# Kernel optimization log

Measured on AMD Instinct MI355X. Metric: run time of the kernel, lower is better.

## Reference

```python
import jax, jax.numpy as jnp
import numpy as np
import math

B, S, HID = 2, 2048, 2048
NH, NKV, HD = 32, 8, 64
THETA = 10000.0
EPS = 1e-6
LAYER_IDX = 1
LAMBDA_INIT = 0.8 - 0.6 * math.exp(-0.3 * LAYER_IDX)
LAMBDA_STD = 0.1


def setup_inputs() -> dict:
    key = jax.random.key(0)
    ks = jax.random.split(key, 10)
    hidden_states = jax.random.normal(ks[0], (B, S, HID), jnp.float32)
    # RoPE cos/sin, llama convention: emb = cat(freqs, freqs)
    inv_freq = 1.0 / (THETA ** (np.arange(0, HD, 2, dtype=np.float32) / HD))
    freqs = np.outer(np.arange(S, dtype=np.float32), inv_freq)  # [S, HD/2]
    emb = np.concatenate([freqs, freqs], axis=-1)                # [S, HD]
    cos = jnp.broadcast_to(jnp.asarray(np.cos(emb), jnp.float32)[None], (B, S, HD))
    sin = jnp.broadcast_to(jnp.asarray(np.sin(emb), jnp.float32)[None], (B, S, HD))
    # additive causal mask [B,1,S,S]
    causal = jnp.triu(jnp.full((S, S), -1e9, dtype=jnp.float32), k=1)
    attention_mask = jnp.broadcast_to(causal[None, None], (B, 1, S, S))
    sc = 0.02
    wq = sc * jax.random.normal(ks[1], (NH * HD, HID), jnp.float32)
    wk = sc * jax.random.normal(ks[2], (NKV * HD, HID), jnp.float32)
    wv = sc * jax.random.normal(ks[3], (NKV * HD, HID), jnp.float32)
    wo = sc * jax.random.normal(ks[4], (HID, NH * HD), jnp.float32)
    lambda_q1 = LAMBDA_STD * jax.random.normal(ks[5], (HD,), jnp.float32)
    lambda_k1 = LAMBDA_STD * jax.random.normal(ks[6], (HD,), jnp.float32)
    lambda_q2 = LAMBDA_STD * jax.random.normal(ks[7], (HD,), jnp.float32)
    lambda_k2 = LAMBDA_STD * jax.random.normal(ks[8], (HD,), jnp.float32)
    return {"hidden_states": hidden_states, "cos": cos, "sin": sin,
            "attention_mask": attention_mask, "wq": wq, "wk": wk, "wv": wv,
            "wo": wo, "lambda_q1": lambda_q1, "lambda_k1": lambda_k1,
            "lambda_q2": lambda_q2, "lambda_k2": lambda_k2}


def _rotate_half(x):
    x1, x2 = jnp.split(x, 2, axis=-1)
    return jnp.concatenate([-x2, x1], axis=-1)


def reference(hidden_states, cos, sin, attention_mask, wq, wk, wv, wo,
              lambda_q1, lambda_k1, lambda_q2, lambda_k2):
    b, s, _ = hidden_states.shape
    # projections -> [b, h, s, d]
    q = jnp.einsum('bsh,oh->bso', hidden_states, wq).reshape(b, s, NH, HD).transpose(0, 2, 1, 3)
    k = jnp.einsum('bsh,oh->bso', hidden_states, wk).reshape(b, s, NKV, HD).transpose(0, 2, 1, 3)
    v = jnp.einsum('bsh,oh->bso', hidden_states, wv).reshape(b, s, NKV, HD).transpose(0, 2, 1, 3)
    # rotary
    c, sn = cos[:, None], sin[:, None]  # [b,1,s,d]
    q = q * c + _rotate_half(q) * sn
    k = k * c + _rotate_half(k) * sn
    # GQA repeat
    groups = NH // NKV
    k = jnp.repeat(k, groups, axis=1)
    v = jnp.repeat(v, groups, axis=1)
    # diff-attention value trick: pair head i with head i+NH/2 -> [b, NH, s, 2d]
    v = jnp.concatenate([v[:, :NH // 2], v[:, NH // 2:]], axis=-1)  # [b, NH/2, s, 2d]
    v = jnp.concatenate([v, v], axis=1)                              # [b, NH, s, 2d]
    # scores + causal mask, stable softmax in fp32
    aw = jnp.einsum('bhqd,bhkd->bhqk', q, k) / math.sqrt(HD)
    aw = aw + attention_mask
    aw = jax.nn.softmax(aw.astype(jnp.float32), axis=-1).astype(q.dtype)
    ao = jnp.einsum('bhqk,bhkd->bhqd', aw, v)  # [b, NH, s, 2d]
    lam1 = jnp.exp(jnp.sum((lambda_q1 * lambda_k1).astype(jnp.float32)))
    lam2 = jnp.exp(jnp.sum((lambda_q2 * lambda_k2).astype(jnp.float32)))
    lam = (lam1 - lam2).astype(q.dtype) + LAMBDA_INIT
    a1, a2 = ao[:, :NH // 2], ao[:, NH // 2:]
    out = a1 - lam * a2  # [b, NH/2, s, 2d]
    # RMSNorm over last dim (no affine)
    out = out * jax.lax.rsqrt(jnp.mean(out * out, axis=-1, keepdims=True) + EPS)
    out = (1.0 - LAMBDA_INIT) * out
    out = out.transpose(0, 2, 1, 3).reshape(b, s, NH * HD)
    return jnp.einsum('bso,ho->bsh', out, wo)
```

## Files before the change

### kernel.cpp

```cpp
#include <hip/hip_runtime.h>

typedef __attribute__((ext_vector_type(8))) short bhalf8;
typedef __attribute__((ext_vector_type(4))) float floatx4;

constexpr int B_ = 2, S_ = 2048, HID_ = 2048, NH_ = 32, NKV_ = 8, HD_ = 64;
constexpr float LAMBDA_INIT_F = 0.35550906759096924f;
constexpr float EPS_ = 1e-6f;
constexpr float QSCALE_ = 0.18033688011112042f;

#define DEVINL __device__ __forceinline__

DEVINL float bf2f(unsigned short u) {
    union { unsigned u; float f; } v; v.u = ((unsigned)u) << 16; return v.f;
}
DEVINL unsigned short f2bf(float f) {
    union { float f; unsigned u; } v; v.f = f;
    unsigned u = v.u;
    return (unsigned short)((u + 0x7fffu + ((u >> 16) & 1u)) >> 16);
}
DEVINL float fexp2(float x) {
#if __has_builtin(__builtin_amdgcn_exp2f)
    return __builtin_amdgcn_exp2f(x);
#else
    return exp2f(x);
#endif
}
DEVINL unsigned pk_bf16(float a, float b) {
#if __has_builtin(__builtin_amdgcn_cvt_pk_bf16_f32)
    typedef __bf16 bf16x2_t __attribute__((ext_vector_type(2)));
    bf16x2_t p = __builtin_amdgcn_cvt_pk_bf16_f32(a, b);
    unsigned r;
    __builtin_memcpy(&r, &p, 4);
    return r;
#else
    return (unsigned)f2bf(a) | ((unsigned)f2bf(b) << 16);
#endif
}
DEVINL void load_lds16(const unsigned short* g, unsigned short* l) {
    __builtin_amdgcn_global_load_lds(
        (const __attribute__((address_space(1))) unsigned int*)g,
        (__attribute__((address_space(3))) unsigned int*)l, 16, 0, 0);
}

__global__ __launch_bounds__(256)
void cvt_all(const float* __restrict__ hs, const float* __restrict__ wq,
             const float* __restrict__ wk, const float* __restrict__ wv,
             const float* __restrict__ wo, unsigned short* __restrict__ hs_bf,
             unsigned short* __restrict__ wcat, unsigned short* __restrict__ wo_bf) {
    const size_t i = (size_t)(blockIdx.x * 256 + threadIdx.x) * 4;
    const float* src;
    unsigned short* dst;
    size_t off;
    float scale = 1.f;
    if (i < 8388608) { src = hs; dst = hs_bf; off = 0; }
    else if (i < 12582912) { src = wq; dst = wcat; off = 8388608; scale = QSCALE_; }
    else if (i < 13631488) { src = wk; dst = wcat + 4194304; off = 12582912; }
    else if (i < 14680064) { src = wv; dst = wcat + 5242880; off = 13631488; }
    else { src = wo; dst = wo_bf; off = 14680064; }
    const size_t k = i - off;
    const float4 v = *(const float4*)(src + k);
    ushort4 o;
    o.x = f2bf(v.x * scale); o.y = f2bf(v.y * scale);
    o.z = f2bf(v.z * scale); o.w = f2bf(v.w * scale);
    *(ushort4*)(dst + k) = o;
}

__global__ void lam_kernel(const float* __restrict__ q1, const float* __restrict__ k1,
                           const float* __restrict__ q2, const float* __restrict__ k2,
                           float* __restrict__ lam) {
    const int l = threadIdx.x;
    float p1 = q1[l] * k1[l];
    float p2 = q2[l] * k2[l];
    #pragma unroll
    for (int off = 1; off < 64; off <<= 1) {
        p1 += __shfl_xor(p1, off, 64);
        p2 += __shfl_xor(p2, off, 64);
    }
    if (l == 0) *lam = expf(p1) - expf(p2) + LAMBDA_INIT_F;
}

__global__ __launch_bounds__(256)
void gemm_qkv(const unsigned short* __restrict__ A, const unsigned short* __restrict__ Bw,
              const float* __restrict__ cosb, const float* __restrict__ sinb,
              unsigned short* __restrict__ Qr, unsigned short* __restrict__ Kr,
              unsigned short* __restrict__ VT) {
    constexpr int K = 2048;
    union GS {
        struct { unsigned short A[2][128][32]; unsigned short B[2][128][32]; } d;
        unsigned short vt[128][130];
    };
    __shared__ __align__(16) GS gsm;
    const int t = threadIdx.x;
    const int w = t >> 6, lane = t & 63, quad = lane >> 4, lid = lane & 15;
    const int wr = (w >> 1) * 64, wc = (w & 1) * 64;
    const long bm = (long)blockIdx.x * 128, bn = (long)blockIdx.y * 128;

    floatx4 acc[4][4];
    #pragma unroll
    for (int i = 0; i < 4; i++)
        #pragma unroll
        for (int j = 0; j < 4; j++) acc[i][j] = (floatx4){0.f, 0.f, 0.f, 0.f};

    const int s0 = t, s1 = t + 256;
    const unsigned short* Ag0 = A + (bm + (s0 >> 2)) * (long)K + (s0 & 3) * 8;
    const unsigned short* Ag1 = A + (bm + (s1 >> 2)) * (long)K + (s1 & 3) * 8;
    const unsigned short* Bg0 = Bw + (bn + (s0 >> 2)) * (long)K + (s0 & 3) * 8;
    const unsigned short* Bg1 = Bw + (bn + (s1 >> 2)) * (long)K + (s1 & 3) * 8;
    const int l0 = s0 * 8, l1 = s1 * 8;

    load_lds16(Ag0, &gsm.d.A[0][0][0] + l0);
    load_lds16(Ag1, &gsm.d.A[0][0][0] + l1);
    load_lds16(Bg0, &gsm.d.B[0][0][0] + l0);
    load_lds16(Bg1, &gsm.d.B[0][0][0] + l1);
    __syncthreads();

    const int nk = K >> 5;
    for (int kt = 0; kt < nk; kt++) {
        const int cur = kt & 1, nxt = cur ^ 1;
        if (kt + 1 < nk) {
            const int off = (kt + 1) << 5;
            load_lds16(Ag0 + off, &gsm.d.A[nxt][0][0] + l0);
            load_lds16(Ag1 + off, &gsm.d.A[nxt][0][0] + l1);
            load_lds16(Bg0 + off, &gsm.d.B[nxt][0][0] + l0);
            load_lds16(Bg1 + off, &gsm.d.B[nxt][0][0] + l1);
        }
        bhalf8 af[4], bf[4];
        #pragma unroll
        for (int i = 0; i < 4; i++) af[i] = *(const bhalf8*)&gsm.d.A[cur][wr + i * 16 + lid][quad * 8];
        #pragma unroll
        for (int j = 0; j < 4; j++) bf[j] = *(const bhalf8*)&gsm.d.B[cur][wc + j * 16 + lid][quad * 8];
        #pragma unroll
        for (int i = 0; i < 4; i++)
            #pragma unroll
            for (int j = 0; j < 4; j++)
                acc[i][j] = __builtin_amdgcn_mfma_f32_16x16x32_bf16(af[i], bf[j], acc[i][j], 0, 0, 0);
        __syncthreads();
    }

    const int y = blockIdx.y;
    if (y < 20) {
        const bool isQ = (y < 16);
        #pragma unroll
        for (int i = 0; i < 4; i++) {
            #pragma unroll
            for (int r = 0; r < 4; r++) {
                const long row = bm + wr + i * 16 + quad * 4 + r;
                const int bb = (int)(row >> 11), s = (int)(row & 2047);
                const float* cp = cosb + (size_t)row * 64;
                const float* sp = sinb + (size_t)row * 64;
                #pragma unroll
                for (int jj = 0; jj < 4; jj++) {
                    const int col = (int)bn + wc + jj * 16 + lid;
                    const int d = col & 63;
                    const float x = acc[i][jj][r];
                    const float oth = acc[i][jj ^ 2][r];
                    const float rot = (jj < 2) ? -oth : oth;
                    const float yv = x * cp[d] + rot * sp[d];
                    if (isQ) {
                        const int h = col >> 6;
                        Qr[((size_t)(bb * NH_ + h) * S_ + s) * HD_ + d] = f2bf(yv);
                    } else {
                        const int h = (col - 2048) >> 6;
                        Kr[((size_t)(bb * NKV_ + h) * S_ + s) * HD_ + d] = f2bf(yv);
                    }
                }
            }
        }
    } else {
        #pragma unroll
        for (int i = 0; i < 4; i++)
            #pragma unroll
            for (int jj = 0; jj < 4; jj++)
                #pragma unroll
                for (int r = 0; r < 4; r++)
                    gsm.vt[wr + i * 16 + quad * 4 + r][wc + jj * 16 + lid] = f2bf(acc[i][jj][r]);
        __syncthreads();
        const int b0 = (int)(bm >> 11), sbase = (int)(bm & 2047);
        #pragma unroll 4
        for (int it = 0; it < 32; it++) {
            const int d = w + 4 * it;
            const int colg = (int)bn + d;
            const int h = (colg - 2560) >> 6;
            const int dl = colg & 63;
            const int sl = lane * 2;
            const unsigned v = (unsigned)gsm.vt[sl][d] | ((unsigned)gsm.vt[sl + 1][d] << 16);
            *(unsigned*)(VT + ((size_t)(b0 * NKV_ + h) * HD_ + dl) * S_ + sbase + sl) = v;
        }
    }
}

__global__ __launch_bounds__(256)
void gemm_bt(const unsigned short* __restrict__ A, const unsigned short* __restrict__ Bw,
             float* __restrict__ Cout, int M, int N, int K) {
    __shared__ __align__(16) unsigned short As[2][128][32];
    __shared__ __align__(16) unsigned short Bs[2][128][32];
    const int t = threadIdx.x;
    const int w = t >> 6, lane = t & 63, quad = lane >> 4, lid = lane & 15;
    const int wr = (w >> 1) * 64, wc = (w & 1) * 64;
    const long bm = (long)blockIdx.x * 128, bn = (long)blockIdx.y * 128;

    floatx4 acc[4][4];
    #pragma unroll
    for (int i = 0; i < 4; i++)
        #pragma unroll
        for (int j = 0; j < 4; j++) acc[i][j] = (floatx4){0.f, 0.f, 0.f, 0.f};

    const int s0 = t, s1 = t + 256;
    const unsigned short* Ag0 = A + (bm + (s0 >> 2)) * (long)K + (s0 & 3) * 8;
    const unsigned short* Ag1 = A + (bm + (s1 >> 2)) * (long)K + (s1 & 3) * 8;
    const unsigned short* Bg0 = Bw + (bn + (s0 >> 2)) * (long)K + (s0 & 3) * 8;
    const unsigned short* Bg1 = Bw + (bn + (s1 >> 2)) * (long)K + (s1 & 3) * 8;
    const int l0 = s0 * 8, l1 = s1 * 8;

    load_lds16(Ag0, &As[0][0][0] + l0);
    load_lds16(Ag1, &As[0][0][0] + l1);
    load_lds16(Bg0, &Bs[0][0][0] + l0);
    load_lds16(Bg1, &Bs[0][0][0] + l1);
    __syncthreads();

    const int nk = K >> 5;
    for (int kt = 0; kt < nk; kt++) {
        const int cur = kt & 1, nxt = cur ^ 1;
        if (kt + 1 < nk) {
            const int off = (kt + 1) << 5;
            load_lds16(Ag0 + off, &As[nxt][0][0] + l0);
            load_lds16(Ag1 + off, &As[nxt][0][0] + l1);
            load_lds16(Bg0 + off, &Bs[nxt][0][0] + l0);
            load_lds16(Bg1 + off, &Bs[nxt][0][0] + l1);
        }
        bhalf8 af[4], bf[4];
        #pragma unroll
        for (int i = 0; i < 4; i++) af[i] = *(const bhalf8*)&As[cur][wr + i * 16 + lid][quad * 8];
        #pragma unroll
        for (int j = 0; j < 4; j++) bf[j] = *(const bhalf8*)&Bs[cur][wc + j * 16 + lid][quad * 8];
        #pragma unroll
        for (int i = 0; i < 4; i++)
            #pragma unroll
            for (int j = 0; j < 4; j++)
                acc[i][j] = __builtin_amdgcn_mfma_f32_16x16x32_bf16(af[i], bf[j], acc[i][j], 0, 0, 0);
        __syncthreads();
    }

    #pragma unroll
    for (int i = 0; i < 4; i++) {
        #pragma unroll
        for (int j = 0; j < 4; j++) {
            const long row = bm + wr + i * 16 + quad * 4;
            const long col = bn + wc + j * 16 + lid;
            #pragma unroll
            for (int r = 0; r < 4; r++) Cout[(row + r) * N + col] = acc[i][j][r];
        }
    }
}

__global__ __launch_bounds__(512, 4)
void attn_diff(const unsigned short* __restrict__ Qr, const unsigned short* __restrict__ Kr,
               const unsigned short* __restrict__ VT, const float* __restrict__ lamp,
               unsigned short* __restrict__ attn) {
    union SM {
        struct {
            unsigned short Kt[2][64][72];
            unsigned short Vt[128][72];
            unsigned short Pt[8][16][72];
        } a;
        unsigned short Ot[2][64][136];
    };
    __shared__ __align__(16) SM sm;

    const int j = blockIdx.y, b = blockIdx.z;
    const int t = threadIdx.x;
    const int w = t >> 6, lane = t & 63, quad = lane >> 4, lid = lane & 15;
    const int st = w >> 2;
    const int rh = (w & 3) * 16;
    const int kv1 = j >> 2, kv2 = 4 + (j >> 2);
    const int qhead = j + st * 16;
    const float lam = *lamp;

    const int ss = t >> 8, kidx = t & 255;
    const int key_s = kidx >> 2, dh = (kidx & 3) * 16;
    const unsigned short* ksrc0 = Kr + (size_t)(b * NKV_ + (ss ? kv2 : kv1)) * S_ * HD_ +
                                  (size_t)key_s * HD_ + dh;
    const int d7 = t >> 2, vh = (t & 3) * 16;
    const unsigned short* vsrc0 = VT + ((size_t)(b * NKV_ + (d7 < 64 ? kv1 : kv2)) * HD_ +
                                        (d7 & 63)) * (size_t)S_ + vh;

    for (int half = 0; half < 2; half++) {
        const int qt = half ? (31 - (int)blockIdx.x) : (int)blockIdx.x;
        const int qb = qt * 64;

        const unsigned short* qbase =
            Qr + ((size_t)((b * NH_ + qhead) * S_) + qb + rh + lid) * HD_;
        const bhalf8 qa0 = *(const bhalf8*)(qbase + quad * 8);
        const bhalf8 qa1 = *(const bhalf8*)(qbase + 32 + quad * 8);

        floatx4 acc[8];
        #pragma unroll
        for (int c = 0; c < 8; c++) acc[c] = (floatx4){0.f, 0.f, 0.f, 0.f};
        float l_acc[4] = {0.f, 0.f, 0.f, 0.f};

        const int nkt = qt + 1;

        for (int kt = 0; kt < nkt; kt++) {
            const int k0 = kt * 64;
            const unsigned short* kp = ksrc0 + (size_t)k0 * HD_;
            const unsigned short* vp = vsrc0 + k0;
            int4 kr0 = *(const int4*)(kp);
            int4 kr1 = *(const int4*)(kp + 8);
            int4 vr0 = *(const int4*)(vp);
            int4 vr1 = *(const int4*)(vp + 8);
            __syncthreads();
            *(int4*)&sm.a.Kt[ss][key_s][dh] = kr0;
            *(int4*)&sm.a.Kt[ss][key_s][dh + 8] = kr1;
            *(int4*)&sm.a.Vt[d7][vh] = vr0;
            *(int4*)&sm.a.Vt[d7][vh + 8] = vr1;
            __syncthreads();

            const bool last = (kt == nkt - 1);
            const int nt_lim = last ? ((w & 3) + 1) : 4;

            floatx4 sc[4];
            #pragma unroll
            for (int nt = 0; nt < 4; nt++) {
                if (nt < nt_lim) {
                    const bhalf8 kb0 = *(const bhalf8*)&sm.a.Kt[st][nt * 16 + lid][quad * 8];
                    const bhalf8 kb1 = *(const bhalf8*)&sm.a.Kt[st][nt * 16 + lid][32 + quad * 8];
                    floatx4 z = (floatx4){0.f, 0.f, 0.f, 0.f};
                    z = __builtin_amdgcn_mfma_f32_16x16x32_bf16(qa0, kb0, z, 0, 0, 0);
                    z = __builtin_amdgcn_mfma_f32_16x16x32_bf16(qa1, kb1, z, 0, 0, 0);
                    sc[nt] = z;
                }
            }

            if (last) {
                #pragma unroll
                for (int nt = 0; nt < 4; nt++) {
                    const int keyg = k0 + nt * 16 + lid;
                    #pragma unroll
                    for (int r = 0; r < 4; r++) {
                        float p = 0.f;
                        if (nt < nt_lim) {
                            const int rowg = qb + rh + quad * 4 + r;
                            p = (keyg > rowg) ? 0.f : fexp2(sc[nt][r]);
                        }
                        sc[nt][r] = p;
                        l_acc[r] += p;
                    }
                }
            } else {
                #pragma unroll
                for (int nt = 0; nt < 4; nt++)
                    #pragma unroll
                    for (int r = 0; r < 4; r++) {
                        const float p = fexp2(sc[nt][r]);
                        sc[nt][r] = p;
                        l_acc[r] += p;
                    }
            }

            #pragma unroll
            for (int nt = 0; nt < 4; nt++) {
                #pragma unroll
                for (int r = 0; r < 4; r += 2) {
                    const unsigned pk = pk_bf16(sc[nt][r], sc[nt][r + 1]);
                    sm.a.Pt[w][quad * 4 + r][nt * 16 + lid] = (unsigned short)(pk & 0xffff);
                    sm.a.Pt[w][quad * 4 + r + 1][nt * 16 + lid] = (unsigned short)(pk >> 16);
                }
            }

            #pragma unroll
            for (int kk = 0; kk < 2; kk++) {
                if (nt_lim > kk * 2) {
                    const bhalf8 pa = *(const bhalf8*)&sm.a.Pt[w][lid][kk * 32 + quad * 8];
                    #pragma unroll
                    for (int c = 0; c < 8; c++) {
                        const bhalf8 vb = *(const bhalf8*)&sm.a.Vt[c * 16 + lid][kk * 32 + quad * 8];
                        acc[c] = __builtin_amdgcn_mfma_f32_16x16x32_bf16(pa, vb, acc[c], 0, 0, 0);
                    }
                }
            }
        }

        #pragma unroll
        for (int off = 1; off < 16; off <<= 1)
            #pragma unroll
            for (int r = 0; r < 4; r++) l_acc[r] += __shfl_xor(l_acc[r], off, 64);

        __syncthreads();
        #pragma unroll
        for (int r = 0; r < 4; r++) {
            const float rl = 1.0f / l_acc[r];
            #pragma unroll
            for (int c = 0; c < 8; c++)
                sm.Ot[st][rh + quad * 4 + r][c * 16 + lid] = f2bf(acc[c][r] * rl);
        }
        __syncthreads();

        const int row = t >> 3, m = t & 7;
        float vals[16];
        float ssum = 0.f;
        #pragma unroll
        for (int c = 0; c < 4; c++) {
            const unsigned long long u0 = *(const unsigned long long*)&sm.Ot[0][row][m * 4 + 32 * c];
            const unsigned long long u1 = *(const unsigned long long*)&sm.Ot[1][row][m * 4 + 32 * c];
            #pragma unroll
            for (int i = 0; i < 4; i++) {
                const float x = bf2f((unsigned short)(u0 >> (16 * i))) -
                                lam * bf2f((unsigned short)(u1 >> (16 * i)));
                vals[c * 4 + i] = x;
                ssum += x * x;
            }
        }
        ssum += __shfl_xor(ssum, 1, 64);
        ssum += __shfl_xor(ssum, 2, 64);
        ssum += __shfl_xor(ssum, 4, 64);
        const float scale = (1.f - LAMBDA_INIT_F) * rsqrtf(ssum * (1.f / 128.f) + EPS_);
        unsigned short* dst = attn + (size_t)(b * S_ + qb + row) * (NH_ * HD_) + j * 128 + m * 4;
        #pragma unroll
        for (int c = 0; c < 4; c++) {
            unsigned short ob[4];
            #pragma unroll
            for (int i = 0; i < 4; i++) ob[i] = f2bf(vals[c * 4 + i] * scale);
            *(unsigned long long*)(dst + 32 * c) = *(const unsigned long long*)ob;
        }
        __syncthreads();
    }
}

extern "C" void kernel_launch(void* const* d_in, const int* in_sizes, int n_in,
                              void* d_out, int out_size, void* d_ws, size_t ws_size,
                              hipStream_t stream) {
    const float* hs   = (const float*)d_in[0];
    const float* cosb = (const float*)d_in[1];
    const float* sinb = (const float*)d_in[2];
    const float* wq   = (const float*)d_in[4];
    const float* wk   = (const float*)d_in[5];
    const float* wv   = (const float*)d_in[6];
    const float* wo   = (const float*)d_in[7];
    const float* lq1  = (const float*)d_in[8];
    const float* lk1  = (const float*)d_in[9];
    const float* lq2  = (const float*)d_in[10];
    const float* lk2  = (const float*)d_in[11];

    unsigned short* p = (unsigned short*)d_ws;
    unsigned short* hs_bf = p;  p += (size_t)4096 * 2048;
    unsigned short* wcat  = p;  p += (size_t)3072 * 2048;
    unsigned short* wo_bf = p;  p += (size_t)2048 * 2048;
    unsigned short* Qr    = p;  p += (size_t)B_ * NH_ * S_ * HD_;
    unsigned short* Kr    = p;  p += (size_t)B_ * NKV_ * S_ * HD_;
    unsigned short* VT    = p;  p += (size_t)B_ * NKV_ * S_ * HD_;
    unsigned short* attnb = p;  p += (size_t)4096 * 2048;
    float* lam = (float*)p;

    cvt_all<<<18432, 256, 0, stream>>>(hs, wq, wk, wv, wo, hs_bf, wcat, wo_bf);
    lam_kernel<<<1, 64, 0, stream>>>(lq1, lk1, lq2, lk2, lam);
    gemm_qkv<<<dim3(32, 24), 256, 0, stream>>>(hs_bf, wcat, cosb, sinb, Qr, Kr, VT);
    attn_diff<<<dim3(16, 16, 2), 512, 0, stream>>>(Qr, Kr, VT, lam, attnb);
    gemm_bt<<<dim3(32, 16), 256, 0, stream>>>(attnb, wo_bf, (float*)d_out, 4096, 2048, 2048);
}
```

Measured before the change: 356.2 us.

## Share K/V tiles across two head pairs per attention block and swap GEMM grid order

The attention kernel now runs 1024 threads per block and processes two adjacent diff-head pairs that share the same KV head. Each K/V tile loaded into shared memory is reused by twice as many waves, which halves global K/V traffic per query head. The epilogue is serialized over the two pairs through the shared Ot buffer. Separately, both GEMMs swap grid x/y so consecutive blocks walk along N for the same M row-block, improving L2 reuse of the A tile. Risks are lower occupancy from 1024-thread blocks, extra barriers in the epilogue, and fewer blocks in the attention grid.

```diff
diff --git a/kernel.cpp b/kernel.cpp
--- a/kernel.cpp
+++ b/kernel.cpp
@@ -93,7 +93,7 @@
     const int t = threadIdx.x;
     const int w = t >> 6, lane = t & 63, quad = lane >> 4, lid = lane & 15;
     const int wr = (w >> 1) * 64, wc = (w & 1) * 64;
-    const long bm = (long)blockIdx.x * 128, bn = (long)blockIdx.y * 128;
+    const long bm = (long)blockIdx.y * 128, bn = (long)blockIdx.x * 128;
 
     floatx4 acc[4][4];
     #pragma unroll
@@ -137,9 +137,9 @@
         __syncthreads();
     }
 
-    const int y = blockIdx.y;
-    if (y < 20) {
-        const bool isQ = (y < 16);
+    const int x = blockIdx.x;
+    if (x < 20) {
+        const bool isQ = (x < 16);
         #pragma unroll
         for (int i = 0; i < 4; i++) {
             #pragma unroll
@@ -152,10 +152,10 @@
                 for (int jj = 0; jj < 4; jj++) {
                     const int col = (int)bn + wc + jj * 16 + lid;
                     const int d = col & 63;
-                    const float x = acc[i][jj][r];
+                    const float xv = acc[i][jj][r];
                     const float oth = acc[i][jj ^ 2][r];
                     const float rot = (jj < 2) ? -oth : oth;
-                    const float yv = x * cp[d] + rot * sp[d];
+                    const float yv = xv * cp[d] + rot * sp[d];
                     if (isQ) {
                         const int h = col >> 6;
                         Qr[((size_t)(bb * NH_ + h) * S_ + s) * HD_ + d] = f2bf(yv);
@@ -197,7 +197,7 @@
     const int t = threadIdx.x;
     const int w = t >> 6, lane = t & 63, quad = lane >> 4, lid = lane & 15;
     const int wr = (w >> 1) * 64, wc = (w & 1) * 64;
-    const long bm = (long)blockIdx.x * 128, bn = (long)blockIdx.y * 128;
+    const long bm = (long)blockIdx.y * 128, bn = (long)blockIdx.x * 128;
 
     floatx4 acc[4][4];
     #pragma unroll
@@ -253,7 +253,7 @@
     }
 }
 
-__global__ __launch_bounds__(512, 4)
+__global__ __launch_bounds__(1024)
 void attn_diff(const unsigned short* __restrict__ Qr, const unsigned short* __restrict__ Kr,
                const unsigned short* __restrict__ VT, const float* __restrict__ lamp,
                unsigned short* __restrict__ attn) {
@@ -261,26 +261,30 @@
         struct {
             unsigned short Kt[2][64][72];
             unsigned short Vt[128][72];
-            unsigned short Pt[8][16][72];
+            unsigned short Pt[16][16][72];
         } a;
         unsigned short Ot[2][64][136];
     };
     __shared__ __align__(16) SM sm;
 
-    const int j = blockIdx.y, b = blockIdx.z;
+    const int by = blockIdx.y, b = blockIdx.z;
     const int t = threadIdx.x;
     const int w = t >> 6, lane = t & 63, quad = lane >> 4, lid = lane & 15;
-    const int st = w >> 2;
-    const int rh = (w & 3) * 16;
-    const int kv1 = j >> 2, kv2 = 4 + (j >> 2);
+    const int st = w & 1;
+    const int jj = (w >> 1) & 1;
+    const int rq = w >> 2;
+    const int rh = rq * 16;
+    const int kvb = by;
+    const int j = by * 2 + jj;
+    const int kv1 = j >> 2, kv2 = 4 + kv1;
     const int qhead = j + st * 16;
     const float lam = *lamp;
 
-    const int ss = t >> 8, kidx = t & 255;
-    const int key_s = kidx >> 2, dh = (kidx & 3) * 16;
+    const int ss = t >> 9;
+    const int key_s = (t >> 3) & 63, dh = (t & 7) * 8;
     const unsigned short* ksrc0 = Kr + (size_t)(b * NKV_ + (ss ? kv2 : kv1)) * S_ * HD_ +
                                   (size_t)key_s * HD_ + dh;
-    const int d7 = t >> 2, vh = (t & 3) * 16;
+    const int d7 = t >> 3, vh = (t & 7) * 8;
     const unsigned short* vsrc0 = VT + ((size_t)(b * NKV_ + (d7 < 64 ? kv1 : kv2)) * HD_ +
                                         (d7 & 63)) * (size_t)S_ + vh;
 
@@ -302,21 +306,15 @@
 
         for (int kt = 0; kt < nkt; kt++) {
             const int k0 = kt * 64;
-            const unsigned short* kp = ksrc0 + (size_t)k0 * HD_;
-            const unsigned short* vp = vsrc0 + k0;
-            int4 kr0 = *(const int4*)(kp);
-            int4 kr1 = *(const int4*)(kp + 8);
-            int4 vr0 = *(const int4*)(vp);
-            int4 vr1 = *(const int4*)(vp + 8);
+            const int4 kr0 = *(const int4*)(ksrc0 + (size_t)k0 * HD_);
+            const int4 vr0 = *(const int4*)(vsrc0 + k0);
             __syncthreads();
             *(int4*)&sm.a.Kt[ss][key_s][dh] = kr0;
-            *(int4*)&sm.a.Kt[ss][key_s][dh + 8] = kr1;
             *(int4*)&sm.a.Vt[d7][vh] = vr0;
-            *(int4*)&sm.a.Vt[d7][vh + 8] = vr1;
             __syncthreads();
 
             const bool last = (kt == nkt - 1);
-            const int nt_lim = last ? ((w & 3) + 1) : 4;
+            const int nt_lim = last ? (rq + 1) : 4;
 
             floatx4 sc[4];
             #pragma unroll
@@ -385,44 +383,50 @@
             #pragma unroll
             for (int r = 0; r < 4; r++) l_acc[r] += __shfl_xor(l_acc[r], off, 64);
 
-        __syncthreads();
-        #pragma unroll
-        for (int r = 0; r < 4; r++) {
-            const float rl = 1.0f / l_acc[r];
-            #pragma unroll
-            for (int c = 0; c < 8; c++)
-                sm.Ot[st][rh + quad * 4 + r][c * 16 + lid] = f2bf(acc[c][r] * rl);
-        }
-        __syncthreads();
-
-        const int row = t >> 3, m = t & 7;
-        float vals[16];
-        float ssum = 0.f;
-        #pragma unroll
-        for (int c = 0; c < 4; c++) {
-            const unsigned long long u0 = *(const unsigned long long*)&sm.Ot[0][row][m * 4 + 32 * c];
-            const unsigned long long u1 = *(const unsigned long long*)&sm.Ot[1][row][m * 4 + 32 * c];
-            #pragma unroll
-            for (int i = 0; i < 4; i++) {
-                const float x = bf2f((unsigned short)(u0 >> (16 * i))) -
-                                lam * bf2f((unsigned short)(u1 >> (16 * i)));
-                vals[c * 4 + i] = x;
-                ssum += x * x;
-            }
-        }
-        ssum += __shfl_xor(ssum, 1, 64);
-        ssum += __shfl_xor(ssum, 2, 64);
-        ssum += __shfl_xor(ssum, 4, 64);
-        const float scale = (1.f - LAMBDA_INIT_F) * rsqrtf(ssum * (1.f / 128.f) + EPS_);
-        unsigned short* dst = attn + (size_t)(b * S_ + qb + row) * (NH_ * HD_) + j * 128 + m * 4;
-        #pragma unroll
-        for (int c = 0; c < 4; c++) {
-            unsigned short ob[4];
-            #pragma unroll
-            for (int i = 0; i < 4; i++) ob[i] = f2bf(vals[c * 4 + i] * scale);
-            *(unsigned long long*)(dst + 32 * c) = *(const unsigned long long*)ob;
-        }
-        __syncthreads();
+        #pragma unroll
+        for (int je = 0; je < 2; je++) {
+            __syncthreads();
+            if (jj == je) {
+                #pragma unroll
+                for (int r = 0; r < 4; r++) {
+                    const float rl = 1.0f / l_acc[r];
+                    #pragma unroll
+                    for (int c = 0; c < 8; c++)
+                        sm.Ot[st][rh + quad * 4 + r][c * 16 + lid] = f2bf(acc[c][r] * rl);
+                }
+            }
+            __syncthreads();
+
+            const int row = t >> 4, m = t & 15;
+            const int d0 = m * 8;
+            float vals[8];
+            float ssum = 0.f;
+            #pragma unroll
+            for (int c = 0; c < 2; c++) {
+                const unsigned long long u0 =
+                    *(const unsigned long long*)&sm.Ot[0][row][d0 + 4 * c];
+                const unsigned long long u1 =
+                    *(const unsigned long long*)&sm.Ot[1][row][d0 + 4 * c];
+                #pragma unroll
+                for (int i = 0; i < 4; i++) {
+                    const float x = bf2f((unsigned short)(u0 >> (16 * i))) -
+                                    lam * bf2f((unsigned short)(u1 >> (16 * i)));
+                    vals[c * 4 + i] = x;
+                    ssum += x * x;
+                }
+            }
+            ssum += __shfl_xor(ssum, 1, 64);
+            ssum += __shfl_xor(ssum, 2, 64);
+            ssum += __shfl_xor(ssum, 4, 64);
+            ssum += __shfl_xor(ssum, 8, 64);
+            const float scale = (1.f - LAMBDA_INIT_F) * rsqrtf(ssum * (1.f / 128.f) + EPS_);
+            unsigned short* dst = attn + (size_t)(b * S_ + qb + row) * (NH_ * HD_) +
+                                  (by * 2 + je) * 128 + d0;
+            unsigned short ob[8];
+            #pragma unroll
+            for (int i = 0; i < 8; i++) ob[i] = f2bf(vals[i] * scale);
+            *(int4*)dst = *(const int4*)ob;
+        }
     }
 }
 
@@ -453,7 +457,7 @@
 
     cvt_all<<<18432, 256, 0, stream>>>(hs, wq, wk, wv, wo, hs_bf, wcat, wo_bf);
     lam_kernel<<<1, 64, 0, stream>>>(lq1, lk1, lq2, lk2, lam);
-    gemm_qkv<<<dim3(32, 24), 256, 0, stream>>>(hs_bf, wcat, cosb, sinb, Qr, Kr, VT);
-    attn_diff<<<dim3(16, 16, 2), 512, 0, stream>>>(Qr, Kr, VT, lam, attnb);
-    gemm_bt<<<dim3(32, 16), 256, 0, stream>>>(attnb, wo_bf, (float*)d_out, 4096, 2048, 2048);
-}
+    gemm_qkv<<<dim3(24, 32), 256, 0, stream>>>(hs_bf, wcat, cosb, sinb, Qr, Kr, VT);
+    attn_diff<<<dim3(16, 8, 2), 1024, 0, stream>>>(Qr, Kr, VT, lam, attnb);
+    gemm_bt<<<dim3(16, 32), 256, 0, stream>>>(attnb, wo_bf, (float*)d_out, 4096, 2048, 2048);
+}
```

Result: no change. 360.3 us (+1.1%).
